# Optimization experiments

Measured on AMD Instinct MI355X. Metric: run time of the kernel, lower is better.

Reference implementation:

```python
import jax, jax.numpy as jnp
import numpy as np

DIM0, DIMO, WIDTH, DEPTH = 64, 16, 128, 6  # depth = number of weight matrices
N = 524288


def setup_inputs() -> dict:
    key = jax.random.key(0)
    ks = jax.random.split(key, DEPTH + 1)
    x = jax.random.normal(ks[0], (N, DIM0), dtype=jnp.float32)
    bd0 = 1.0 / np.sqrt(DIM0)   # first layer init bound (per torch code)
    bd = 1.0 / np.sqrt(WIDTH)   # remaining layers init bound
    W0 = jax.random.uniform(ks[1], (DIM0, WIDTH), minval=-bd0, maxval=bd0, dtype=jnp.float32)
    W1 = jax.random.uniform(ks[2], (WIDTH, WIDTH), minval=-bd, maxval=bd, dtype=jnp.float32)
    W2 = jax.random.uniform(ks[3], (WIDTH, WIDTH), minval=-bd, maxval=bd, dtype=jnp.float32)
    W3 = jax.random.uniform(ks[4], (WIDTH, WIDTH), minval=-bd, maxval=bd, dtype=jnp.float32)
    W4 = jax.random.uniform(ks[5], (WIDTH, WIDTH), minval=-bd, maxval=bd, dtype=jnp.float32)
    W5 = jax.random.uniform(ks[6], (WIDTH, DIMO), minval=-bd, maxval=bd, dtype=jnp.float32)
    bias = jnp.zeros((DIMO,), dtype=jnp.float32)
    return {"x": x, "W0": W0, "W1": W1, "W2": W2, "W3": W3, "W4": W4, "W5": W5, "bias": bias}


def reference(x, W0, W1, W2, W3, W4, W5, bias):
    # Fully-fused MLP math: matmul (no bias) + ReLU for every layer except the
    # last (output_activation='None'); then cast back to x dtype and add bias.
    h = jax.nn.relu(x @ W0)
    h = jax.nn.relu(h @ W1)
    h = jax.nn.relu(h @ W2)
    h = jax.nn.relu(h @ W3)
    h = jax.nn.relu(h @ W4)
    out = (h @ W5).astype(x.dtype) + bias
    return out
```

## Files before the change

### kernel.cpp

```cpp
#include <hip/hip_runtime.h>
#include <stdint.h>


typedef __bf16 bf16x8 __attribute__((ext_vector_type(8)));
typedef __bf16 bf16x4 __attribute__((ext_vector_type(4)));
typedef float  floatx4 __attribute__((ext_vector_type(4)));

#define GAS __attribute__((address_space(1)))
#define LAS __attribute__((address_space(3)))

constexpr int NS   = 524288;
constexpr int TILE = 128;
constexpr int NBLK = NS / TILE;

constexpr int WTOT = 9472;

__global__ void prep_weights(const float* __restrict__ W0, const float* __restrict__ W1,
                             const float* __restrict__ W2, const float* __restrict__ W3,
                             const float* __restrict__ W4, const float* __restrict__ W5,
                             bf16x8* __restrict__ ws) {
  int gid = blockIdx.x * blockDim.x + threadIdx.x;
  if (gid >= WTOT) return;
  const float* Wsrc; int nout, cpr, base;
  if (gid < 1024)      { Wsrc = W0; nout = 128; cpr = 8;  base = 0;    }
  else if (gid < 3072) { Wsrc = W1; nout = 128; cpr = 16; base = 1024; }
  else if (gid < 5120) { Wsrc = W2; nout = 128; cpr = 16; base = 3072; }
  else if (gid < 7168) { Wsrc = W3; nout = 128; cpr = 16; base = 5120; }
  else if (gid < 9216) { Wsrc = W4; nout = 128; cpr = 16; base = 7168; }
  else                 { Wsrc = W5; nout = 16;  cpr = 16; base = 9216; }
  int id = gid - base;
  int n  = id / cpr;
  int p  = id % cpr;
  int c  = p ^ (n & 7);
  bf16x8 v;
#pragma unroll
  for (int j = 0; j < 8; ++j)
    v[j] = (__bf16)Wsrc[(8 * c + j) * nout + n];
  ws[gid] = v;
}

__device__ __forceinline__ void stage_w(const bf16x8* __restrict__ src, bf16x8* dst,
                                        int nchunks, int w, int lane) {
  int per  = nchunks >> 2;
  int base = w * per;
  for (int i = 0; i < per; i += 64) {
    __builtin_amdgcn_global_load_lds(
        (const GAS void*)(src + base + i + lane),
        (LAS void*)(dst + base + i),
        16, 0, 0);
  }
}

__device__ __forceinline__ void zero_acc(floatx4 acc[4][4]) {
  floatx4 z = {0.f, 0.f, 0.f, 0.f};
#pragma unroll
  for (int i = 0; i < 4; ++i)
#pragma unroll
    for (int j = 0; j < 4; ++j) acc[i][j] = z;
}

template <int KT, int CPR>
__device__ __forceinline__ void layer_mm(const bf16x8* Wb, const bf16x8* Hb,
                                         floatx4 acc[4][4], int m_base, int n_base,
                                         int l15, int g) {
#pragma unroll
  for (int kt = 0; kt < KT; ++kt) {
    const int cx = (kt * 4 + g) ^ (l15 & 7);
    bf16x8 a[4], b[4];
#pragma unroll
    for (int i = 0; i < 4; ++i) a[i] = Wb[(m_base + 16 * i + l15) * CPR + cx];
#pragma unroll
    for (int i = 0; i < 4; ++i) b[i] = Hb[(n_base + 16 * i + l15) * 16 + cx];
#pragma unroll
    for (int ot = 0; ot < 4; ++ot)
#pragma unroll
      for (int nt = 0; nt < 4; ++nt)
        acc[ot][nt] = __builtin_amdgcn_mfma_f32_16x16x32_bf16(a[ot], b[nt], acc[ot][nt], 0, 0, 0);
  }
}

__device__ __forceinline__ void write_h(bf16x4* H8, const floatx4 acc[4][4],
                                        int m_base, int n_base, int l15, int g) {
#pragma unroll
  for (int ot = 0; ot < 4; ++ot) {
    int ob    = m_base + 16 * ot + 4 * g;
    int phys8 = (((ob >> 3) ^ (l15 & 7)) << 1) | ((ob >> 2) & 1);
#pragma unroll
    for (int nt = 0; nt < 4; ++nt) {
      int s = n_base + 16 * nt + l15;
      floatx4 v = acc[ot][nt];
      bf16x4 h;
      h[0] = (__bf16)fmaxf(v[0], 0.0f);
      h[1] = (__bf16)fmaxf(v[1], 0.0f);
      h[2] = (__bf16)fmaxf(v[2], 0.0f);
      h[3] = (__bf16)fmaxf(v[3], 0.0f);
      H8[s * 32 + phys8] = h;
    }
  }
}

__global__ void __launch_bounds__(256) mlp_kernel(const float* __restrict__ x,
                                                  const float* __restrict__ bias,
                                                  const bf16x8* __restrict__ wimg,
                                                  float* __restrict__ out) {
  __shared__ bf16x8 Hbuf[TILE * 16];
  __shared__ bf16x8 Wbuf[2048];

  const int t    = threadIdx.x;
  const int lane = t & 63;
  const int w    = t >> 6;
  const int l15  = lane & 15;
  const int g    = lane >> 4;
  const int m_base = (w & 1) * 64;
  const int n_base = (w >> 1) * 64;
  const int tile = blockIdx.x;

  constexpr int WOFF[6] = {0, 1024, 3072, 5120, 7168, 9216};
  constexpr int WCNT[6] = {1024, 2048, 2048, 2048, 2048, 256};

  stage_w(wimg + WOFF[0], Wbuf, WCNT[0], w, lane);

  const float* xt = x + (size_t)tile * TILE * 64;
#pragma unroll
  for (int i = 0; i < 4; ++i) {
    int f2 = t + 256 * i;
    int s = f2 >> 3, c = f2 & 7;
    const floatx4* src = (const floatx4*)(xt + f2 * 8);
    floatx4 lo = src[0], hi = src[1];
    bf16x8 v;
    v[0] = (__bf16)lo[0]; v[1] = (__bf16)lo[1]; v[2] = (__bf16)lo[2]; v[3] = (__bf16)lo[3];
    v[4] = (__bf16)hi[0]; v[5] = (__bf16)hi[1]; v[6] = (__bf16)hi[2]; v[7] = (__bf16)hi[3];
    Hbuf[s * 16 + (c ^ (s & 7))] = v;
  }
  __syncthreads();

  floatx4 acc[4][4];

  zero_acc(acc);
  layer_mm<2, 8>(Wbuf, Hbuf, acc, m_base, n_base, l15, g);
  __syncthreads();
  stage_w(wimg + WOFF[1], Wbuf, WCNT[1], w, lane);
  write_h((bf16x4*)Hbuf, acc, m_base, n_base, l15, g);
  __syncthreads();

#pragma unroll
  for (int l = 1; l <= 4; ++l) {
    zero_acc(acc);
    layer_mm<4, 16>(Wbuf, Hbuf, acc, m_base, n_base, l15, g);
    __syncthreads();
    stage_w(wimg + WOFF[l + 1], Wbuf, WCNT[l + 1], w, lane);
    write_h((bf16x4*)Hbuf, acc, m_base, n_base, l15, g);
    __syncthreads();
  }

  floatx4 a5[2];
  {
    floatx4 z = {0.f, 0.f, 0.f, 0.f};
    a5[0] = z; a5[1] = z;
  }
  const int n5 = w * 32;
#pragma unroll
  for (int kt = 0; kt < 4; ++kt) {
    int cx = (kt * 4 + g) ^ (l15 & 7);
    bf16x8 a = Wbuf[l15 * 16 + cx];
#pragma unroll
    for (int nt = 0; nt < 2; ++nt) {
      bf16x8 b = Hbuf[(n5 + 16 * nt + l15) * 16 + cx];
      a5[nt] = __builtin_amdgcn_mfma_f32_16x16x32_bf16(a, b, a5[nt], 0, 0, 0);
    }
  }
  floatx4 bv = *(const floatx4*)(bias + 4 * g);
  floatx4* outv = (floatx4*)out;
#pragma unroll
  for (int nt = 0; nt < 2; ++nt) {
    int s = tile * TILE + n5 + 16 * nt + l15;
    outv[s * 4 + g] = a5[nt] + bv;
  }
}

extern "C" void kernel_launch(void* const* d_in, const int* in_sizes, int n_in,
                              void* d_out, int out_size, void* d_ws, size_t ws_size,
                              hipStream_t stream) {
  (void)in_sizes; (void)n_in; (void)out_size; (void)ws_size;
  const float* x    = (const float*)d_in[0];
  const float* W0   = (const float*)d_in[1];
  const float* W1   = (const float*)d_in[2];
  const float* W2   = (const float*)d_in[3];
  const float* W3   = (const float*)d_in[4];
  const float* W4   = (const float*)d_in[5];
  const float* W5   = (const float*)d_in[6];
  const float* bias = (const float*)d_in[7];
  bf16x8* ws = (bf16x8*)d_ws;

  prep_weights<<<(WTOT + 255) / 256, 256, 0, stream>>>(W0, W1, W2, W3, W4, W5, ws);
  mlp_kernel<<<NBLK, 256, 0, stream>>>(x, bias, (const bf16x8*)ws, (float*)d_out);
}
```

Measured before the change: 267.6 us.

## Load MFMA weight fragments directly from global memory instead of staging in LDS

```diff
diff --git a/kernel.cpp b/kernel.cpp
--- a/kernel.cpp
+++ b/kernel.cpp
@@ -5,9 +5,6 @@
 typedef __bf16 bf16x8 __attribute__((ext_vector_type(8)));
 typedef __bf16 bf16x4 __attribute__((ext_vector_type(4)));
 typedef float  floatx4 __attribute__((ext_vector_type(4)));
-
-#define GAS __attribute__((address_space(1)))
-#define LAS __attribute__((address_space(3)))
 
 constexpr int NS   = 524288;
 constexpr int TILE = 128;
@@ -21,34 +18,27 @@
                              bf16x8* __restrict__ ws) {
   int gid = blockIdx.x * blockDim.x + threadIdx.x;
   if (gid >= WTOT) return;
-  const float* Wsrc; int nout, cpr, base;
-  if (gid < 1024)      { Wsrc = W0; nout = 128; cpr = 8;  base = 0;    }
-  else if (gid < 3072) { Wsrc = W1; nout = 128; cpr = 16; base = 1024; }
-  else if (gid < 5120) { Wsrc = W2; nout = 128; cpr = 16; base = 3072; }
-  else if (gid < 7168) { Wsrc = W3; nout = 128; cpr = 16; base = 5120; }
-  else if (gid < 9216) { Wsrc = W4; nout = 128; cpr = 16; base = 7168; }
-  else                 { Wsrc = W5; nout = 16;  cpr = 16; base = 9216; }
-  int id = gid - base;
-  int n  = id / cpr;
-  int p  = id % cpr;
-  int c  = p ^ (n & 7);
+  const float* Wsrc; int nout, KT, base;
+  if (gid < 1024)      { Wsrc = W0; nout = 128; KT = 2; base = 0;    }
+  else if (gid < 3072) { Wsrc = W1; nout = 128; KT = 4; base = 1024; }
+  else if (gid < 5120) { Wsrc = W2; nout = 128; KT = 4; base = 3072; }
+  else if (gid < 7168) { Wsrc = W3; nout = 128; KT = 4; base = 5120; }
+  else if (gid < 9216) { Wsrc = W4; nout = 128; KT = 4; base = 7168; }
+  else                 { Wsrc = W5; nout = 16;  KT = 4; base = 9216; }
+  int id  = gid - base;
+  int p   = id & 63;
+  int l15 = p & 15;
+  int g   = p >> 4;
+  int blk = id >> 6;
+  int kt  = blk % KT;
+  int it  = blk / KT;
+  int row = it * 16 + l15;
+  int kc  = kt * 4 + g;
   bf16x8 v;
 #pragma unroll
   for (int j = 0; j < 8; ++j)
-    v[j] = (__bf16)Wsrc[(8 * c + j) * nout + n];
+    v[j] = (__bf16)Wsrc[(8 * kc + j) * nout + row];
   ws[gid] = v;
-}
-
-__device__ __forceinline__ void stage_w(const bf16x8* __restrict__ src, bf16x8* dst,
-                                        int nchunks, int w, int lane) {
-  int per  = nchunks >> 2;
-  int base = w * per;
-  for (int i = 0; i < per; i += 64) {
-    __builtin_amdgcn_global_load_lds(
-        (const GAS void*)(src + base + i + lane),
-        (LAS void*)(dst + base + i),
-        16, 0, 0);
-  }
 }
 
 __device__ __forceinline__ void zero_acc(floatx4 acc[4][4]) {
@@ -59,16 +49,16 @@
     for (int j = 0; j < 4; ++j) acc[i][j] = z;
 }
 
-template <int KT, int CPR>
-__device__ __forceinline__ void layer_mm(const bf16x8* Wb, const bf16x8* Hb,
-                                         floatx4 acc[4][4], int m_base, int n_base,
-                                         int l15, int g) {
+template <int KT>
+__device__ __forceinline__ void layer_mm(const bf16x8* __restrict__ wg,
+                                         const bf16x8* Hb, floatx4 acc[4][4],
+                                         int n_base, int l15, int g, int lane) {
 #pragma unroll
   for (int kt = 0; kt < KT; ++kt) {
     const int cx = (kt * 4 + g) ^ (l15 & 7);
     bf16x8 a[4], b[4];
 #pragma unroll
-    for (int i = 0; i < 4; ++i) a[i] = Wb[(m_base + 16 * i + l15) * CPR + cx];
+    for (int i = 0; i < 4; ++i) a[i] = wg[((i * KT + kt) << 6) + lane];
 #pragma unroll
     for (int i = 0; i < 4; ++i) b[i] = Hb[(n_base + 16 * i + l15) * 16 + cx];
 #pragma unroll
@@ -99,26 +89,21 @@
   }
 }
 
-__global__ void __launch_bounds__(256) mlp_kernel(const float* __restrict__ x,
-                                                  const float* __restrict__ bias,
-                                                  const bf16x8* __restrict__ wimg,
-                                                  float* __restrict__ out) {
+__global__ void __launch_bounds__(256, 4) mlp_kernel(const float* __restrict__ x,
+                                                     const float* __restrict__ bias,
+                                                     const bf16x8* __restrict__ wimg,
+                                                     float* __restrict__ out) {
   __shared__ bf16x8 Hbuf[TILE * 16];
-  __shared__ bf16x8 Wbuf[2048];
 
   const int t    = threadIdx.x;
   const int lane = t & 63;
   const int w    = t >> 6;
   const int l15  = lane & 15;
   const int g    = lane >> 4;
-  const int m_base = (w & 1) * 64;
+  const int m_half = w & 1;
+  const int m_base = m_half * 64;
   const int n_base = (w >> 1) * 64;
   const int tile = blockIdx.x;
-
-  constexpr int WOFF[6] = {0, 1024, 3072, 5120, 7168, 9216};
-  constexpr int WCNT[6] = {1024, 2048, 2048, 2048, 2048, 256};
-
-  stage_w(wimg + WOFF[0], Wbuf, WCNT[0], w, lane);
 
   const float* xt = x + (size_t)tile * TILE * 64;
 #pragma unroll
@@ -137,18 +122,17 @@
   floatx4 acc[4][4];
 
   zero_acc(acc);
-  layer_mm<2, 8>(Wbuf, Hbuf, acc, m_base, n_base, l15, g);
+  layer_mm<2>(wimg + m_half * 512, Hbuf, acc, n_base, l15, g, lane);
   __syncthreads();
-  stage_w(wimg + WOFF[1], Wbuf, WCNT[1], w, lane);
   write_h((bf16x4*)Hbuf, acc, m_base, n_base, l15, g);
   __syncthreads();
 
+  constexpr int WOFF[5] = {1024, 3072, 5120, 7168, 9216};
 #pragma unroll
-  for (int l = 1; l <= 4; ++l) {
+  for (int l = 0; l < 4; ++l) {
     zero_acc(acc);
-    layer_mm<4, 16>(Wbuf, Hbuf, acc, m_base, n_base, l15, g);
+    layer_mm<4>(wimg + WOFF[l] + m_half * 1024, Hbuf, acc, n_base, l15, g, lane);
     __syncthreads();
-    stage_w(wimg + WOFF[l + 1], Wbuf, WCNT[l + 1], w, lane);
     write_h((bf16x4*)Hbuf, acc, m_base, n_base, l15, g);
     __syncthreads();
   }
@@ -162,7 +146,7 @@
 #pragma unroll
   for (int kt = 0; kt < 4; ++kt) {
     int cx = (kt * 4 + g) ^ (l15 & 7);
-    bf16x8 a = Wbuf[l15 * 16 + cx];
+    bf16x8 a = wimg[9216 + (kt << 6) + lane];
 #pragma unroll
     for (int nt = 0; nt < 2; ++nt) {
       bf16x8 b = Hbuf[(n5 + 16 * nt + l15) * 16 + cx];
```

New measurement: 282.7 us. +5.6%, slower.
